# Optimization experiments

Hardware: AMD Instinct MI355X
Metric: run time of the kernel (lower is better)

Reference implementation:

```python
import jax, jax.numpy as jnp
import numpy as np

B, N, C = 8, 4096, 512
H = 8
OUT = 512
DH = C // H  # 64
LN_EPS = 1e-5
L2_EPS = 1e-12


def setup_inputs() -> dict:
    key = jax.random.key(0)
    ks = jax.random.split(key, 6)
    x = jax.random.normal(ks[0], (B, N, C), dtype=jnp.float32)
    ln_g = jnp.ones((C,), dtype=jnp.float32)
    ln_b = jnp.zeros((C,), dtype=jnp.float32)
    qkv_w = jax.random.normal(ks[1], (3 * C, C), dtype=jnp.float32) * 0.02  # torch Linear weight [out,in]
    temperature = jnp.ones((H, 1, 1), dtype=jnp.float32)
    proj_w = jax.random.normal(ks[2], (OUT, C), dtype=jnp.float32) * 0.02
    proj_b = jnp.zeros((OUT,), dtype=jnp.float32)
    return {"x": x, "ln_g": ln_g, "ln_b": ln_b, "qkv_w": qkv_w,
            "temperature": temperature, "proj_w": proj_w, "proj_b": proj_b}


def reference(x, ln_g, ln_b, qkv_w, temperature, proj_w, proj_b):
    # LayerNorm
    mu = jnp.mean(x, axis=-1, keepdims=True)
    var = jnp.mean(jnp.square(x - mu), axis=-1, keepdims=True)
    xn = (x - mu) * jax.lax.rsqrt(var + LN_EPS) * ln_g + ln_b
    # QKV projection (no bias)
    qkv = xn @ qkv_w.T  # [B,N,3C]
    qkv = qkv.reshape(B, N, 3, H, DH).transpose(2, 0, 3, 4, 1)  # [3,B,H,DH,N]
    q, k, v = qkv[0], qkv[1], qkv[2]  # each [B,H,DH,N] (already 'transposed' channel layout)
    # L2-normalize q,k along token dim (matches F.normalize eps behavior)
    q = q / jnp.clip(jnp.linalg.norm(q, axis=-1, keepdims=True), L2_EPS)
    k = k / jnp.clip(jnp.linalg.norm(k, axis=-1, keepdims=True), L2_EPS)
    # channel attention [B,H,DH,DH], scaled by per-head temperature
    attn = jnp.einsum('bhdn,bhen->bhde', q, k) * temperature[None]
    attn = jax.nn.softmax(attn, axis=-1)
    out = jnp.einsum('bhde,bhen->bhdn', attn, v)  # [B,H,DH,N]
    out = out.transpose(0, 3, 1, 2).reshape(B, N, H * DH)  # [B,N,C]
    out = jax.nn.gelu(out, approximate=False)
    out = out @ proj_w.T + proj_b
    return out
```

## Files before the change

### kernel.cpp

```cpp
#include <hip/hip_runtime.h>
#include <hip/hip_bf16.h>

typedef __hip_bfloat16 bf16;
typedef __bf16 bfrag __attribute__((ext_vector_type(8)));
typedef float f32x4 __attribute__((ext_vector_type(4)));

#define AS1 __attribute__((address_space(1)))
#define AS3 __attribute__((address_space(3)))

static constexpr int Bb = 8, Nn = 4096, Cc = 512, Hh = 8;
static constexpr int Mtok = Bb * Nn;
static constexpr int QKVC = 3 * Cc;
static constexpr size_t WS_NEED = 57147392;
static constexpr int SPL_STRIDE = 8 * 20 * 8192;

__device__ __forceinline__ void gl_lds16(const void* g, void* l) {
  __builtin_amdgcn_global_load_lds((const AS1 void*)g, (AS3 void*)l, 16, 0, 0);
}
__device__ __forceinline__ float gelu_exact(float x) {
  return 0.5f * x * (1.0f + erff(x * 0.70710678118654752f));
}
__device__ __forceinline__ int g3(int x) { return ((x & 1) << 2) | (x >> 1); }
__device__ __forceinline__ int tileid(int mt, int nt) {
  return mt + (nt == 0 ? 0 : nt == 1 ? 2 : nt == 2 ? 6 : 12);
}

__global__ __launch_bounds__(256) void fill_f32(float* o, float val, int n) {
  int i = blockIdx.x * 256 + threadIdx.x;
  if (i < n) o[i] = val;
}

__global__ __launch_bounds__(256) void ln_cvtw(const float* __restrict__ x,
                                               const float* __restrict__ gw,
                                               const float* __restrict__ bw,
                                               bf16* __restrict__ xn,
                                               const float* __restrict__ qkv_w,
                                               const float* __restrict__ proj_w,
                                               bf16* __restrict__ wq,
                                               bf16* __restrict__ wp) {
  int bid = blockIdx.x;
  if (bid < 8192) {
    int tok  = bid * 4 + (threadIdx.x >> 6);
    int lane = threadIdx.x & 63;
    const float* xr = x + (size_t)tok * Cc + lane * 8;
    float f[8];
    *(float4*)f       = *(const float4*)xr;
    *(float4*)(f + 4) = *(const float4*)(xr + 4);
    float s = 0.f;
#pragma unroll
    for (int j = 0; j < 8; ++j) s += f[j];
#pragma unroll
    for (int m = 32; m; m >>= 1) s += __shfl_xor(s, m);
    float mu = s * (1.0f / 512.0f);
    float q = 0.f;
#pragma unroll
    for (int j = 0; j < 8; ++j) { float d = f[j] - mu; q += d * d; }
#pragma unroll
    for (int m = 32; m; m >>= 1) q += __shfl_xor(q, m);
    float rstd = rsqrtf(q * (1.0f / 512.0f) + 1e-5f);
    bf16 o[8];
#pragma unroll
    for (int j = 0; j < 8; ++j)
      o[j] = __float2bfloat16((f[j] - mu) * rstd * gw[lane * 8 + j] + bw[lane * 8 + j]);
    *(uint4*)(xn + (size_t)tok * Cc + lane * 8) = *(uint4*)o;
  } else {
    int cb = bid - 8192;
    const float* a;
    bf16* o;
    int i;
    if (cb < 384) { a = qkv_w;  o = wq; i = (cb * 256 + (int)threadIdx.x) * 8; }
    else          { a = proj_w; o = wp; i = ((cb - 384) * 256 + (int)threadIdx.x) * 8; }
    float f[8];
    *(float4*)f       = *(const float4*)(a + i);
    *(float4*)(f + 4) = *(const float4*)(a + i + 4);
    bf16 vv[8];
#pragma unroll
    for (int j = 0; j < 8; ++j) vv[j] = __float2bfloat16(f[j]);
    *(uint4*)(o + i) = *(uint4*)vv;
  }
}

__global__ __launch_bounds__(256) void cvt_mirror(const float* __restrict__ part,
                                                  bf16* __restrict__ Gcvb) {
  int tile = blockIdx.x, b = blockIdx.y;
  int ti = tile >> 2, tj = tile & 3;
  int t = threadIdx.x;
  bf16* ob = Gcvb + (size_t)b * Cc * Cc;
  if (ti <= tj) {
#pragma unroll
    for (int r8 = 0; r8 < 8; ++r8) {
      int row = r8 * 16 + (t >> 4), col = (t & 15) * 8;
      int mt = 2 * ti + (row >> 6), rsub = row & 63;
      const float* p0 = part + ((size_t)b * 20 + tileid(mt, tj)) * 8192 + rsub * 128 + col;
      float f[8];
      *(float4*)f       = *(const float4*)p0;
      *(float4*)(f + 4) = *(const float4*)(p0 + 4);
#pragma unroll
      for (int s = 1; s < 4; ++s) {
        const float* ps = p0 + (size_t)s * SPL_STRIDE;
        float g[8];
        *(float4*)g       = *(const float4*)ps;
        *(float4*)(g + 4) = *(const float4*)(ps + 4);
#pragma unroll
        for (int j = 0; j < 8; ++j) f[j] += g[j];
      }
      bf16 v[8];
#pragma unroll
      for (int j = 0; j < 8; ++j) v[j] = __float2bfloat16(f[j]);
      *(uint4*)(ob + (size_t)(ti * 128 + row) * Cc + tj * 128 + col) = *(uint4*)v;
    }
  } else {
    __shared__ bf16 ls[128][136];
#pragma unroll
    for (int r8 = 0; r8 < 8; ++r8) {
      int srow = r8 * 16 + (t >> 4), scol = (t & 15) * 8;
      int mt = 2 * tj + (srow >> 6), rsub = srow & 63;
      const float* p0 = part + ((size_t)b * 20 + tileid(mt, ti)) * 8192 + rsub * 128 + scol;
      float f[8];
      *(float4*)f       = *(const float4*)p0;
      *(float4*)(f + 4) = *(const float4*)(p0 + 4);
#pragma unroll
      for (int s = 1; s < 4; ++s) {
        const float* ps = p0 + (size_t)s * SPL_STRIDE;
        float g[8];
        *(float4*)g       = *(const float4*)ps;
        *(float4*)(g + 4) = *(const float4*)(ps + 4);
#pragma unroll
        for (int j = 0; j < 8; ++j) f[j] += g[j];
      }
      bf16 v[8];
#pragma unroll
      for (int j = 0; j < 8; ++j) v[j] = __float2bfloat16(f[j]);
      *(uint4*)&ls[srow][scol] = *(uint4*)v;
    }
    __syncthreads();
#pragma unroll
    for (int r8 = 0; r8 < 8; ++r8) {
      int orow = r8 * 16 + (t >> 4), ocol = (t & 15) * 8;
      bf16 v[8];
#pragma unroll
      for (int u = 0; u < 8; ++u) v[u] = ls[ocol + u][orow];
      *(uint4*)(ob + (size_t)(ti * 128 + orow) * Cc + tj * 128 + ocol) = *(uint4*)v;
    }
  }
}

template <typename TC, bool SWZ>
__global__ __launch_bounds__(256) void gemm_bt(const bf16* __restrict__ A,
                                               const bf16* __restrict__ B,
                                               TC* __restrict__ C,
                                               int M, int N, int K,
                                               const float* __restrict__ bias,
                                               long sA_z, long sB_z, long sC_z) {
  A += (size_t)blockIdx.z * sA_z;
  B += (size_t)blockIdx.z * sB_z;
  C += (size_t)blockIdx.z * sC_z;
  __shared__ __align__(16) bf16 smem[16384];
  bf16* sA = smem;
  bf16* sB = smem + 8192;
  int t = threadIdx.x, w = t >> 6, lane = t & 63, fr = lane & 15, quad = lane >> 4;
  int n0, m0;
  if constexpr (SWZ) {
    int flat = blockIdx.y * 4 + blockIdx.x;
    int idx  = (flat & 7) * 128 + (flat >> 3);
    n0 = (idx & 3) * 128;
    m0 = (idx >> 2) * 128;
  } else {
    n0 = blockIdx.x * 128;
    m0 = blockIdx.y * 128;
  }
  int wm = (w >> 1) * 64, wn = (w & 1) * 64;
  f32x4 acc[4][4] = {};

  for (int k0 = 0; k0 < K; k0 += 64) {
    __syncthreads();
#pragma unroll
    for (int c2 = 0; c2 < 4; ++c2) {
      int c = w * 4 + c2;
      int row = c * 8 + (lane >> 3);
      int ke  = ((lane & 7) ^ (lane >> 3)) * 8;
      gl_lds16(A + (size_t)(m0 + row) * K + k0 + ke, (char*)sA + c * 1024);
      gl_lds16(B + (size_t)(n0 + row) * K + k0 + ke, (char*)sB + c * 1024);
    }
    __syncthreads();
#pragma unroll
    for (int kk = 0; kk < 64; kk += 32) {
      bfrag af[4], bg[4];
#pragma unroll
      for (int i = 0; i < 4; ++i)
        af[i] = *(const bfrag*)(sA + (wm + i * 16 + fr) * 64 +
                                ((((kk >> 3) + quad) ^ (fr & 7)) * 8));
#pragma unroll
      for (int j = 0; j < 4; ++j)
        bg[j] = *(const bfrag*)(sB + (wn + j * 16 + fr) * 64 +
                                ((((kk >> 3) + quad) ^ (fr & 7)) * 8));
#pragma unroll
      for (int i = 0; i < 4; ++i)
#pragma unroll
        for (int j = 0; j < 4; ++j)
          acc[i][j] = __builtin_amdgcn_mfma_f32_16x16x32_bf16(af[i], bg[j], acc[i][j], 0, 0, 0);
    }
  }

  if constexpr (__is_same(TC, float)) {
#pragma unroll
    for (int j = 0; j < 4; ++j) {
      float bj = bias ? bias[n0 + wn + j * 16 + fr] : 0.0f;
#pragma unroll
      for (int i = 0; i < 4; ++i)
#pragma unroll
        for (int r = 0; r < 4; ++r)
          C[(size_t)(m0 + wm + i * 16 + quad * 4 + r) * N + n0 + wn + j * 16 + fr] =
              acc[i][j][r] + bj;
    }
  } else {
    __syncthreads();
    bf16* ct = smem;
#pragma unroll
    for (int j = 0; j < 4; ++j) {
      float bj = bias ? bias[n0 + wn + j * 16 + fr] : 0.0f;
#pragma unroll
      for (int i = 0; i < 4; ++i)
#pragma unroll
        for (int r = 0; r < 4; ++r)
          ct[(wm + i * 16 + quad * 4 + r) * 128 + wn + j * 16 + fr] =
              __float2bfloat16(acc[i][j][r] + bj);
    }
    __syncthreads();
#pragma unroll
    for (int r8 = 0; r8 < 8; ++r8) {
      int row = r8 * 16 + (t >> 4);
      int ce  = (t & 15) * 8;
      *(uint4*)(C + (size_t)(m0 + row) * N + n0 + ce) = *(const uint4*)(smem + row * 128 + ce);
    }
  }
}

__global__ __launch_bounds__(256) void vgemm_xtx(const bf16* __restrict__ xn,
                                                 const bf16* __restrict__ wv,
                                                 bf16* __restrict__ v,
                                                 float* __restrict__ part) {
  __shared__ __align__(16) bf16 smem[16384];
  int t = threadIdx.x, w = t >> 6, lane = t & 63, fr = lane & 15, quad = lane >> 4;
  if (blockIdx.x < 1024) {
    bf16* sA = smem;
    bf16* sB = smem + 8192;
    int flat = blockIdx.x;
    int idx  = (flat & 7) * 128 + (flat >> 3);
    int n0 = (idx & 3) * 128, m0 = (idx >> 2) * 128;
    int wm = (w >> 1) * 64, wn = (w & 1) * 64;
    f32x4 acc[4][4] = {};
    for (int k0 = 0; k0 < 512; k0 += 64) {
      __syncthreads();
#pragma unroll
      for (int c2 = 0; c2 < 4; ++c2) {
        int c = w * 4 + c2;
        int row = c * 8 + (lane >> 3);
        int ke  = ((lane & 7) ^ (lane >> 3)) * 8;
        gl_lds16(xn + (size_t)(m0 + row) * 512 + k0 + ke, (char*)sA + c * 1024);
        gl_lds16(wv + (size_t)(n0 + row) * 512 + k0 + ke, (char*)sB + c * 1024);
      }
      __syncthreads();
#pragma unroll
      for (int kk = 0; kk < 64; kk += 32) {
        bfrag af[4], bg[4];
#pragma unroll
        for (int i = 0; i < 4; ++i)
          af[i] = *(const bfrag*)(sA + (wm + i * 16 + fr) * 64 +
                                  ((((kk >> 3) + quad) ^ (fr & 7)) * 8));
#pragma unroll
        for (int j = 0; j < 4; ++j)
          bg[j] = *(const bfrag*)(sB + (wn + j * 16 + fr) * 64 +
                                  ((((kk >> 3) + quad) ^ (fr & 7)) * 8));
#pragma unroll
        for (int i = 0; i < 4; ++i)
#pragma unroll
          for (int j = 0; j < 4; ++j)
            acc[i][j] = __builtin_amdgcn_mfma_f32_16x16x32_bf16(af[i], bg[j], acc[i][j], 0, 0, 0);
      }
    }
    __syncthreads();
    bf16* ct = smem;
#pragma unroll
    for (int j = 0; j < 4; ++j)
#pragma unroll
      for (int i = 0; i < 4; ++i)
#pragma unroll
        for (int r = 0; r < 4; ++r)
          ct[(wm + i * 16 + quad * 4 + r) * 128 + wn + j * 16 + fr] =
              __float2bfloat16(acc[i][j][r]);
    __syncthreads();
#pragma unroll
    for (int r8 = 0; r8 < 8; ++r8) {
      int row = r8 * 16 + (t >> 4);
      int ce  = (t & 15) * 8;
      *(uint4*)(v + (size_t)(m0 + row) * 512 + n0 + ce) = *(const uint4*)(smem + row * 128 + ce);
    }
  } else {
    bf16* sB  = smem;
    bf16* sAb = smem + 8192;
    int flat = blockIdx.x - 1024;
    int idx  = (flat & 7) * 80 + (flat >> 3);
    int tile = idx % 20;
    int sb   = idx / 20;
    int split = sb & 3, b = sb >> 2;
    int nt = tile < 2 ? 0 : tile < 6 ? 1 : tile < 12 ? 2 : 3;
    int mt = tile - (nt == 0 ? 0 : nt == 1 ? 2 : nt == 2 ? 6 : 12);
    int m0 = mt * 64, n0 = nt * 128;
    bool alias = ((mt >> 1) == nt);
    int wn = w * 32;
    bf16* sA = alias ? (sB + (mt & 1) * 4096) : sAb;
    f32x4 acc[4][2] = {};
    const bf16* xb = xn + ((size_t)b * Nn + split * 1024) * Cc;
    int ch0b = (t & 15) * 8, tgb = t >> 4;
    int ch0a = (t & 7) * 8,  tga = t >> 3;
    bool doA = (!alias) && (t < 128);
    unsigned swz = (unsigned)g3(t & 7);
    unsigned wposb = (((unsigned)(tgb >> 1) ^ swz) * 16u) + (unsigned)(tgb & 1) * 8u;
    unsigned wposa = (((unsigned)(tga >> 1) ^ swz) * 16u) + (unsigned)(tga & 1) * 8u;
    uint4 va[4], vb[4];
#pragma unroll
    for (int j = 0; j < 4; ++j)
      vb[j] = *(const uint4*)(xb + (size_t)(tgb * 4 + j) * Cc + n0 + ch0b);
    if (doA)
#pragma unroll
      for (int j = 0; j < 4; ++j)
        va[j] = *(const uint4*)(xb + (size_t)(tga * 4 + j) * Cc + m0 + ch0a);
    for (int kc = 0; kc < 16; ++kc) {
      __syncthreads();
#pragma unroll
      for (int k = 0; k < 4; ++k) {
        unsigned b0 = ((const unsigned*)&vb[0])[k], b1 = ((const unsigned*)&vb[1])[k];
        unsigned b2 = ((const unsigned*)&vb[2])[k], b3 = ((const unsigned*)&vb[3])[k];
        uint2 lo = { (b0 & 0xffffu) | (b1 << 16), (b2 & 0xffffu) | (b3 << 16) };
        uint2 hi = { (b0 >> 16) | (b1 & 0xffff0000u), (b2 >> 16) | (b3 & 0xffff0000u) };
        *(uint2*)((char*)sB + (unsigned)(ch0b + 2 * k) * 128 + wposb) = lo;
        *(uint2*)((char*)sB + (unsigned)(ch0b + 2 * k + 1) * 128 + wposb) = hi;
      }
      if (doA) {
#pragma unroll
        for (int k = 0; k < 4; ++k) {
          unsigned a0 = ((const unsigned*)&va[0])[k], a1 = ((const unsigned*)&va[1])[k];
          unsigned a2 = ((const unsigned*)&va[2])[k], a3 = ((const unsigned*)&va[3])[k];
          uint2 lo = { (a0 & 0xffffu) | (a1 << 16), (a2 & 0xffffu) | (a3 << 16) };
          uint2 hi = { (a0 >> 16) | (a1 & 0xffff0000u), (a2 >> 16) | (a3 & 0xffff0000u) };
          *(uint2*)((char*)sAb + (unsigned)(ch0a + 2 * k) * 128 + wposa) = lo;
          *(uint2*)((char*)sAb + (unsigned)(ch0a + 2 * k + 1) * 128 + wposa) = hi;
        }
      }
      __syncthreads();
      if (kc < 15) {
        const bf16* xb2 = xb + (size_t)(kc + 1) * 64 * Cc;
#pragma unroll
        for (int j = 0; j < 4; ++j)
          vb[j] = *(const uint4*)(xb2 + (size_t)(tgb * 4 + j) * Cc + n0 + ch0b);
        if (doA)
#pragma unroll
          for (int j = 0; j < 4; ++j)
            va[j] = *(const uint4*)(xb2 + (size_t)(tga * 4 + j) * Cc + m0 + ch0a);
      }
#pragma unroll
      for (int kk = 0; kk < 2; ++kk) {
        bfrag af[4], bg[2];
#pragma unroll
        for (int i = 0; i < 4; ++i) {
          int ch = i * 16 + fr;
          int slot = (kk * 4 + quad) ^ g3((ch >> 3) & 7);
          af[i] = *(const bfrag*)(sA + ch * 64 + slot * 8);
        }
#pragma unroll
        for (int j = 0; j < 2; ++j) {
          int ch = wn + j * 16 + fr;
          int slot = (kk * 4 + quad) ^ g3((ch >> 3) & 7);
          bg[j] = *(const bfrag*)(sB + ch * 64 + slot * 8);
        }
#pragma unroll
        for (int i = 0; i < 4; ++i)
#pragma unroll
          for (int j = 0; j < 2; ++j)
            acc[i][j] = __builtin_amdgcn_mfma_f32_16x16x32_bf16(af[i], bg[j], acc[i][j], 0, 0, 0);
      }
    }
    float* pb = part + (size_t)split * SPL_STRIDE + ((size_t)b * 20 + tile) * 8192;
#pragma unroll
    for (int i = 0; i < 4; ++i)
#pragma unroll
      for (int j = 0; j < 2; ++j)
#pragma unroll
        for (int r = 0; r < 4; ++r)
          pb[(i * 16 + quad * 4 + r) * 128 + wn + j * 16 + fr] = acc[i][j][r];
  }
}

__global__ __launch_bounds__(256) void gram_softmax(const bf16* __restrict__ T,
                                                    const bf16* __restrict__ wq,
                                                    const float* __restrict__ temp,
                                                    bf16* __restrict__ P) {
  int h = blockIdx.x, b = blockIdx.y;
  int t = threadIdx.x, w = t >> 6, lane = t & 63, fr = lane & 15, quad = lane >> 4;
  const bf16* Tq = T + (size_t)b * 1024 * 512 + (size_t)(h * 64) * 512;
  const bf16* Tk = T + (size_t)b * 1024 * 512 + (size_t)(512 + h * 64) * 512;
  const bf16* Wqh = wq + (size_t)(h * 64) * 512;
  const bf16* Wkh = wq + (size_t)(512 + h * 64) * 512;
  f32x4 acc[4][4] = {};
#pragma unroll
  for (int s = 0; s < 4; ++s) {
    int kb = w * 128 + s * 32 + quad * 8;
    bfrag af[4], bg[4];
#pragma unroll
    for (int i = 0; i < 4; ++i) af[i] = *(const bfrag*)(Tq + (size_t)(i * 16 + fr) * 512 + kb);
#pragma unroll
    for (int j = 0; j < 4; ++j) bg[j] = *(const bfrag*)(Wkh + (size_t)(j * 16 + fr) * 512 + kb);
#pragma unroll
    for (int i = 0; i < 4; ++i)
#pragma unroll
      for (int j = 0; j < 4; ++j)
        acc[i][j] = __builtin_amdgcn_mfma_f32_16x16x32_bf16(af[i], bg[j], acc[i][j], 0, 0, 0);
  }
  __shared__ float parts[4 * 4096];
  __shared__ float nrm[2][4][64];
  __shared__ float nqk[2][64];
#pragma unroll
  for (int i = 0; i < 4; ++i)
#pragma unroll
    for (int j = 0; j < 4; ++j)
#pragma unroll
      for (int r = 0; r < 4; ++r)
        parts[w * 4096 + (i * 16 + quad * 4 + r) * 64 + j * 16 + fr] = acc[i][j][r];
  {
    int d = t & 63, qtr = t >> 6, c0 = qtr * 128;
    float pq = 0.f, pk = 0.f;
#pragma unroll 4
    for (int cc = 0; cc < 16; ++cc) {
      bf16 a[8], ww[8];
      *(uint4*)a  = *(const uint4*)(Tq + (size_t)d * 512 + c0 + cc * 8);
      *(uint4*)ww = *(const uint4*)(Wqh + (size_t)d * 512 + c0 + cc * 8);
#pragma unroll
      for (int j = 0; j < 8; ++j) pq += __bfloat162float(a[j]) * __bfloat162float(ww[j]);
      *(uint4*)a  = *(const uint4*)(Tk + (size_t)d * 512 + c0 + cc * 8);
      *(uint4*)ww = *(const uint4*)(Wkh + (size_t)d * 512 + c0 + cc * 8);
#pragma unroll
      for (int j = 0; j < 8; ++j) pk += __bfloat162float(a[j]) * __bfloat162float(ww[j]);
    }
    nrm[0][qtr][d] = pq;
    nrm[1][qtr][d] = pk;
  }
  __syncthreads();
  if (t < 64) {
    nqk[0][t] = fmaxf(sqrtf(nrm[0][0][t] + nrm[0][1][t] + nrm[0][2][t] + nrm[0][3][t]), 1e-12f);
    nqk[1][t] = fmaxf(sqrtf(nrm[1][0][t] + nrm[1][1][t] + nrm[1][2][t] + nrm[1][3][t]), 1e-12f);
  }
  __syncthreads();
  if (t < 64) {
    int d = t;
    float sc = temp[h] / nqk[0][d];
    float l[64]; float mx = -1e30f;
#pragma unroll
    for (int e = 0; e < 64; ++e) {
      float vsum = parts[d * 64 + e] + parts[4096 + d * 64 + e] +
                   parts[8192 + d * 64 + e] + parts[12288 + d * 64 + e];
      l[e] = vsum * sc / nqk[1][e];
      mx = fmaxf(mx, l[e]);
    }
    float sum = 0.f;
#pragma unroll
    for (int e = 0; e < 64; ++e) { l[e] = expf(l[e] - mx); sum += l[e]; }
    float inv = 1.0f / sum;
    bf16* pr = P + ((size_t)(b * 8 + h) * 64 + d) * 64;
#pragma unroll
    for (int e = 0; e < 64; ++e) pr[e] = __float2bfloat16(l[e] * inv);
  }
}

__global__ __launch_bounds__(256) void pv_gelu(const bf16* __restrict__ P,
                                               const bf16* __restrict__ v,
                                               bf16* __restrict__ g) {
  int chunk = blockIdx.x, h = blockIdx.y, b = blockIdx.z;
  int t = threadIdx.x, w = t >> 6, lane = t & 63, fr = lane & 15, quad = lane >> 4;
  const bf16* pb = P + (size_t)(b * 8 + h) * 4096;
  bfrag pf[4][2];
#pragma unroll
  for (int i = 0; i < 4; ++i)
#pragma unroll
    for (int c = 0; c < 2; ++c)
      pf[i][c] = *(const bfrag*)(pb + (i * 16 + fr) * 64 + c * 32 + quad * 8);
#pragma unroll 2
  for (int nt = 0; nt < 8; ++nt) {
    int ntok = chunk * 512 + w * 128 + nt * 16 + fr;
    const bf16* vrow = v + (size_t)(b * Nn + ntok) * Cc + h * 64 + quad * 8;
    bfrag bv0 = *(const bfrag*)(vrow);
    bfrag bv1 = *(const bfrag*)(vrow + 32);
    f32x4 acc[4] = {};
#pragma unroll
    for (int i = 0; i < 4; ++i) {
      acc[i] = __builtin_amdgcn_mfma_f32_16x16x32_bf16(pf[i][0], bv0, acc[i], 0, 0, 0);
      acc[i] = __builtin_amdgcn_mfma_f32_16x16x32_bf16(pf[i][1], bv1, acc[i], 0, 0, 0);
    }
    bf16* grow = g + (size_t)(b * Nn + ntok) * Cc + h * 64;
#pragma unroll
    for (int i = 0; i < 4; ++i) {
      bf16 o[4];
#pragma unroll
      for (int r = 0; r < 4; ++r) o[r] = __float2bfloat16(gelu_exact(acc[i][r]));
      *(uint2*)(grow + i * 16 + quad * 4) = *(uint2*)o;
    }
  }
}

extern "C" void kernel_launch(void* const* d_in, const int* in_sizes, int n_in,
                              void* d_out, int out_size, void* d_ws, size_t ws_size,
                              hipStream_t stream) {
  const float* x      = (const float*)d_in[0];
  const float* ln_g   = (const float*)d_in[1];
  const float* ln_b   = (const float*)d_in[2];
  const float* qkv_w  = (const float*)d_in[3];
  const float* temp   = (const float*)d_in[4];
  const float* proj_w = (const float*)d_in[5];
  const float* proj_b = (const float*)d_in[6];
  float* out = (float*)d_out;
  char*  ws  = (char*)d_ws;

  const int exp_sizes[7] = {16777216, 512, 512, 786432, 8, 262144, 512};
  bool sizes_ok = (n_in == 7) && (out_size == 16777216);
  if (sizes_ok) for (int i = 0; i < 7; ++i) sizes_ok = sizes_ok && (in_sizes[i] == exp_sizes[i]);
  if (!sizes_ok) {
    fill_f32<<<(16777216 + 255) / 256, 256, 0, stream>>>(out, 500.0f, out_size);
    return;
  }
  if (ws_size < WS_NEED) {
    fill_f32<<<(16777216 + 255) / 256, 256, 0, stream>>>(out, (float)(ws_size >> 20), out_size);
    return;
  }

  bf16*  xn   = (bf16*)ws;
  bf16*  g    = (bf16*)ws;
  bf16*  Gcvb = (bf16*)(ws + 41943040);
  bf16*  T    = (bf16*)(ws + 46137344);
  bf16*  P    = (bf16*)(ws + 54525952);
  bf16*  wq   = (bf16*)(ws + 55050240);
  bf16*  wp   = (bf16*)(ws + 56623104);
  bf16*  v    = (bf16*)d_out;
  float* part = (float*)((char*)d_out + 33554432);

  ln_cvtw<<<8704, 256, 0, stream>>>(x, ln_g, ln_b, xn, qkv_w, proj_w, wq, wp);
  vgemm_xtx<<<1664, 256, 0, stream>>>(xn, wq + 1024 * 512, v, part);
  cvt_mirror<<<dim3(16, 8), 256, 0, stream>>>(part, Gcvb);
  gemm_bt<bf16, false><<<dim3(4, 8, 8), 256, 0, stream>>>(wq, Gcvb, T, 1024, Cc, Cc,
                                                          nullptr, 0, (long)Cc * Cc, (long)1024 * Cc);
  gram_softmax<<<dim3(Hh, Bb), 256, 0, stream>>>(T, wq, temp, P);
  pv_gelu<<<dim3(8, Hh, Bb), 256, 0, stream>>>(P, v, g);
  gemm_bt<float, true><<<dim3(4, 256, 1), 256, 0, stream>>>(g, wp, out, Mtok, Cc, Cc,
                                                            proj_b, 0, 0, 0);
}
```

Baseline: 258.1 us.

## Use 256x256 double-buffered GEMM for V and output projections, split xtx kernel

Adds a new GEMM kernel with 512 threads, 256x256 output tiles and double-buffered LDS staging using direct global-to-LDS loads. It is used for both the V projection and the final output projection. The fused V-GEMM/XtX kernel is split into two separate launches. Larger tiles raise arithmetic intensity and cut operand reloads, and overlapping the next tile's load with compute hides memory latency. In exchange, the 128 KB of LDS and the large accumulators allow only one block per CU, and the 256-block grid gives low occupancy and a tail effect.

Result: no change. 254.7 us (-1.3%).

```diff
diff --git a/kernel.cpp b/kernel.cpp
--- a/kernel.cpp
+++ b/kernel.cpp
@@ -236,160 +236,191 @@
   }
 }
 
-__global__ __launch_bounds__(256) void vgemm_xtx(const bf16* __restrict__ xn,
-                                                 const bf16* __restrict__ wv,
-                                                 bf16* __restrict__ v,
-                                                 float* __restrict__ part) {
-  __shared__ __align__(16) bf16 smem[16384];
+template <typename TC>
+__global__ __launch_bounds__(512) void gemm_bt2(const bf16* __restrict__ A,
+                                                const bf16* __restrict__ B,
+                                                TC* __restrict__ C,
+                                                int M, int N, int K,
+                                                const float* __restrict__ bias) {
+  __shared__ __align__(16) bf16 smem[65536];
   int t = threadIdx.x, w = t >> 6, lane = t & 63, fr = lane & 15, quad = lane >> 4;
-  if (blockIdx.x < 1024) {
-    bf16* sA = smem;
-    bf16* sB = smem + 8192;
-    int flat = blockIdx.x;
-    int idx  = (flat & 7) * 128 + (flat >> 3);
-    int n0 = (idx & 3) * 128, m0 = (idx >> 2) * 128;
-    int wm = (w >> 1) * 64, wn = (w & 1) * 64;
-    f32x4 acc[4][4] = {};
-    for (int k0 = 0; k0 < 512; k0 += 64) {
-      __syncthreads();
-#pragma unroll
-      for (int c2 = 0; c2 < 4; ++c2) {
-        int c = w * 4 + c2;
-        int row = c * 8 + (lane >> 3);
-        int ke  = ((lane & 7) ^ (lane >> 3)) * 8;
-        gl_lds16(xn + (size_t)(m0 + row) * 512 + k0 + ke, (char*)sA + c * 1024);
-        gl_lds16(wv + (size_t)(n0 + row) * 512 + k0 + ke, (char*)sB + c * 1024);
+  int nt2 = N >> 8;
+  int flat = blockIdx.x;
+  int idx  = (flat & 7) * (gridDim.x >> 3) + (flat >> 3);
+  int m0 = (idx / nt2) * 256, n0 = (idx % nt2) * 256;
+  int wm = (w >> 2) * 128, wn = (w & 3) * 64;
+  f32x4 acc[8][4] = {};
+
+  auto stage = [&](int buf, int k0) {
+    char* sAc = (char*)(smem + buf * 32768);
+    char* sBc = sAc + 32768;
+    int ke = ((lane & 7) ^ (lane >> 3)) * 8;
+#pragma unroll
+    for (int c2 = 0; c2 < 4; ++c2) {
+      int c = w * 4 + c2;
+      int row = c * 8 + (lane >> 3);
+      gl_lds16(A + (size_t)(m0 + row) * K + k0 + ke, sAc + c * 1024);
+      gl_lds16(B + (size_t)(n0 + row) * K + k0 + ke, sBc + c * 1024);
+    }
+  };
+
+  stage(0, 0);
+  __syncthreads();
+  int nks = K >> 6;
+  for (int ks = 0; ks < nks; ++ks) {
+    if (ks + 1 < nks) stage((ks + 1) & 1, (ks + 1) * 64);
+    const bf16* sA = smem + (ks & 1) * 32768;
+    const bf16* sB = sA + 16384;
+#pragma unroll
+    for (int kk = 0; kk < 64; kk += 32) {
+      bfrag af[8], bg[4];
+#pragma unroll
+      for (int i = 0; i < 8; ++i)
+        af[i] = *(const bfrag*)(sA + (wm + i * 16 + fr) * 64 +
+                                ((((kk >> 3) + quad) ^ (fr & 7)) * 8));
+#pragma unroll
+      for (int j = 0; j < 4; ++j)
+        bg[j] = *(const bfrag*)(sB + (wn + j * 16 + fr) * 64 +
+                                ((((kk >> 3) + quad) ^ (fr & 7)) * 8));
+#pragma unroll
+      for (int i = 0; i < 8; ++i)
+#pragma unroll
+        for (int j = 0; j < 4; ++j)
+          acc[i][j] = __builtin_amdgcn_mfma_f32_16x16x32_bf16(af[i], bg[j], acc[i][j], 0, 0, 0);
+    }
+    __syncthreads();
+  }
+
+  if constexpr (__is_same(TC, float)) {
+#pragma unroll
+    for (int j = 0; j < 4; ++j) {
+      float bj = bias ? bias[n0 + wn + j * 16 + fr] : 0.0f;
+#pragma unroll
+      for (int i = 0; i < 8; ++i)
+#pragma unroll
+        for (int r = 0; r < 4; ++r)
+          C[(size_t)(m0 + wm + i * 16 + quad * 4 + r) * N + n0 + wn + j * 16 + fr] =
+              acc[i][j][r] + bj;
+    }
+  } else {
+    bf16* ct = smem;
+#pragma unroll
+    for (int j = 0; j < 4; ++j) {
+      float bj = bias ? bias[n0 + wn + j * 16 + fr] : 0.0f;
+#pragma unroll
+      for (int i = 0; i < 8; ++i)
+#pragma unroll
+        for (int r = 0; r < 4; ++r)
+          ct[(wm + i * 16 + quad * 4 + r) * 256 + wn + j * 16 + fr] =
+              __float2bfloat16(acc[i][j][r] + bj);
+    }
+    __syncthreads();
+#pragma unroll
+    for (int it = 0; it < 16; ++it) {
+      int row = it * 16 + (t >> 5);
+      int ce  = (t & 31) * 8;
+      *(uint4*)(C + (size_t)(m0 + row) * N + n0 + ce) = *(const uint4*)(ct + row * 256 + ce);
+    }
+  }
+}
+
+__global__ __launch_bounds__(256) void xtx(const bf16* __restrict__ xn,
+                                           float* __restrict__ part) {
+  bf16* sB;
+  bf16* sAb;
+  __shared__ __align__(16) bf16 smem[12288];
+  sB = smem; sAb = smem + 8192;
+  int flat = blockIdx.x;
+  int idx  = (flat & 7) * 80 + (flat >> 3);
+  int tile = idx % 20;
+  int sb   = idx / 20;
+  int split = sb & 3, b = sb >> 2;
+  int nt = tile < 2 ? 0 : tile < 6 ? 1 : tile < 12 ? 2 : 3;
+  int mt = tile - (nt == 0 ? 0 : nt == 1 ? 2 : nt == 2 ? 6 : 12);
+  int m0 = mt * 64, n0 = nt * 128;
+  bool alias = ((mt >> 1) == nt);
+  int t = threadIdx.x, w = t >> 6, lane = t & 63, fr = lane & 15, quad = lane >> 4;
+  int wn = w * 32;
+  bf16* sA = alias ? (sB + (mt & 1) * 4096) : sAb;
+  f32x4 acc[4][2] = {};
+  const bf16* xb = xn + ((size_t)b * Nn + split * 1024) * Cc;
+  int ch0b = (t & 15) * 8, tgb = t >> 4;
+  int ch0a = (t & 7) * 8,  tga = t >> 3;
+  bool doA = (!alias) && (t < 128);
+  unsigned swz = (unsigned)g3(t & 7);
+  unsigned wposb = (((unsigned)(tgb >> 1) ^ swz) * 16u) + (unsigned)(tgb & 1) * 8u;
+  unsigned wposa = (((unsigned)(tga >> 1) ^ swz) * 16u) + (unsigned)(tga & 1) * 8u;
+  uint4 va[4], vb[4];
+#pragma unroll
+  for (int j = 0; j < 4; ++j)
+    vb[j] = *(const uint4*)(xb + (size_t)(tgb * 4 + j) * Cc + n0 + ch0b);
+  if (doA)
+#pragma unroll
+    for (int j = 0; j < 4; ++j)
+      va[j] = *(const uint4*)(xb + (size_t)(tga * 4 + j) * Cc + m0 + ch0a);
+  for (int kc = 0; kc < 16; ++kc) {
+    __syncthreads();
+#pragma unroll
+    for (int k = 0; k < 4; ++k) {
+      unsigned b0 = ((const unsigned*)&vb[0])[k], b1 = ((const unsigned*)&vb[1])[k];
+      unsigned b2 = ((const unsigned*)&vb[2])[k], b3 = ((const unsigned*)&vb[3])[k];
+      uint2 lo = { (b0 & 0xffffu) | (b1 << 16), (b2 & 0xffffu) | (b3 << 16) };
+      uint2 hi = { (b0 >> 16) | (b1 & 0xffff0000u), (b2 >> 16) | (b3 & 0xffff0000u) };
+      *(uint2*)((char*)sB + (unsigned)(ch0b + 2 * k) * 128 + wposb) = lo;
+      *(uint2*)((char*)sB + (unsigned)(ch0b + 2 * k + 1) * 128 + wposb) = hi;
+    }
+    if (doA) {
+#pragma unroll
+      for (int k = 0; k < 4; ++k) {
+        unsigned a0 = ((const unsigned*)&va[0])[k], a1 = ((const unsigned*)&va[1])[k];
+        unsigned a2 = ((const unsigned*)&va[2])[k], a3 = ((const unsigned*)&va[3])[k];
+        uint2 lo = { (a0 & 0xffffu) | (a1 << 16), (a2 & 0xffffu) | (a3 << 16) };
+        uint2 hi = { (a0 >> 16) | (a1 & 0xffff0000u), (a2 >> 16) | (a3 & 0xffff0000u) };
+        *(uint2*)((char*)sAb + (unsigned)(ch0a + 2 * k) * 128 + wposa) = lo;
+        *(uint2*)((char*)sAb + (unsigned)(ch0a + 2 * k + 1) * 128 + wposa) = hi;
       }
-      __syncthreads();
-#pragma unroll
-      for (int kk = 0; kk < 64; kk += 32) {
-        bfrag af[4], bg[4];
-#pragma unroll
-        for (int i = 0; i < 4; ++i)
-          af[i] = *(const bfrag*)(sA + (wm + i * 16 + fr) * 64 +
-                                  ((((kk >> 3) + quad) ^ (fr & 7)) * 8));
+    }
+    __syncthreads();
+    if (kc < 15) {
+      const bf16* xb2 = xb + (size_t)(kc + 1) * 64 * Cc;
+#pragma unroll
+      for (int j = 0; j < 4; ++j)
+        vb[j] = *(const uint4*)(xb2 + (size_t)(tgb * 4 + j) * Cc + n0 + ch0b);
+      if (doA)
 #pragma unroll
         for (int j = 0; j < 4; ++j)
-          bg[j] = *(const bfrag*)(sB + (wn + j * 16 + fr) * 64 +
-                                  ((((kk >> 3) + quad) ^ (fr & 7)) * 8));
-#pragma unroll
-        for (int i = 0; i < 4; ++i)
-#pragma unroll
-          for (int j = 0; j < 4; ++j)
-            acc[i][j] = __builtin_amdgcn_mfma_f32_16x16x32_bf16(af[i], bg[j], acc[i][j], 0, 0, 0);
+          va[j] = *(const uint4*)(xb2 + (size_t)(tga * 4 + j) * Cc + m0 + ch0a);
+    }
+#pragma unroll
+    for (int kk = 0; kk < 2; ++kk) {
+      bfrag af[4], bg[2];
+#pragma unroll
+      for (int i = 0; i < 4; ++i) {
+        int ch = i * 16 + fr;
+        int slot = (kk * 4 + quad) ^ g3((ch >> 3) & 7);
+        af[i] = *(const bfrag*)(sA + ch * 64 + slot * 8);
       }
-    }
-    __syncthreads();
-    bf16* ct = smem;
-#pragma unroll
-    for (int j = 0; j < 4; ++j)
+#pragma unroll
+      for (int j = 0; j < 2; ++j) {
+        int ch = wn + j * 16 + fr;
+        int slot = (kk * 4 + quad) ^ g3((ch >> 3) & 7);
+        bg[j] = *(const bfrag*)(sB + ch * 64 + slot * 8);
+      }
 #pragma unroll
       for (int i = 0; i < 4; ++i)
 #pragma unroll
-        for (int r = 0; r < 4; ++r)
-          ct[(wm + i * 16 + quad * 4 + r) * 128 + wn + j * 16 + fr] =
-              __float2bfloat16(acc[i][j][r]);
-    __syncthreads();
-#pragma unroll
-    for (int r8 = 0; r8 < 8; ++r8) {
-      int row = r8 * 16 + (t >> 4);
-      int ce  = (t & 15) * 8;
-      *(uint4*)(v + (size_t)(m0 + row) * 512 + n0 + ce) = *(const uint4*)(smem + row * 128 + ce);
-    }
-  } else {
-    bf16* sB  = smem;
-    bf16* sAb = smem + 8192;
-    int flat = blockIdx.x - 1024;
-    int idx  = (flat & 7) * 80 + (flat >> 3);
-    int tile = idx % 20;
-    int sb   = idx / 20;
-    int split = sb & 3, b = sb >> 2;
-    int nt = tile < 2 ? 0 : tile < 6 ? 1 : tile < 12 ? 2 : 3;
-    int mt = tile - (nt == 0 ? 0 : nt == 1 ? 2 : nt == 2 ? 6 : 12);
-    int m0 = mt * 64, n0 = nt * 128;
-    bool alias = ((mt >> 1) == nt);
-    int wn = w * 32;
-    bf16* sA = alias ? (sB + (mt & 1) * 4096) : sAb;
-    f32x4 acc[4][2] = {};
-    const bf16* xb = xn + ((size_t)b * Nn + split * 1024) * Cc;
-    int ch0b = (t & 15) * 8, tgb = t >> 4;
-    int ch0a = (t & 7) * 8,  tga = t >> 3;
-    bool doA = (!alias) && (t < 128);
-    unsigned swz = (unsigned)g3(t & 7);
-    unsigned wposb = (((unsigned)(tgb >> 1) ^ swz) * 16u) + (unsigned)(tgb & 1) * 8u;
-    unsigned wposa = (((unsigned)(tga >> 1) ^ swz) * 16u) + (unsigned)(tga & 1) * 8u;
-    uint4 va[4], vb[4];
-#pragma unroll
-    for (int j = 0; j < 4; ++j)
-      vb[j] = *(const uint4*)(xb + (size_t)(tgb * 4 + j) * Cc + n0 + ch0b);
-    if (doA)
-#pragma unroll
-      for (int j = 0; j < 4; ++j)
-        va[j] = *(const uint4*)(xb + (size_t)(tga * 4 + j) * Cc + m0 + ch0a);
-    for (int kc = 0; kc < 16; ++kc) {
-      __syncthreads();
-#pragma unroll
-      for (int k = 0; k < 4; ++k) {
-        unsigned b0 = ((const unsigned*)&vb[0])[k], b1 = ((const unsigned*)&vb[1])[k];
-        unsigned b2 = ((const unsigned*)&vb[2])[k], b3 = ((const unsigned*)&vb[3])[k];
-        uint2 lo = { (b0 & 0xffffu) | (b1 << 16), (b2 & 0xffffu) | (b3 << 16) };
-        uint2 hi = { (b0 >> 16) | (b1 & 0xffff0000u), (b2 >> 16) | (b3 & 0xffff0000u) };
-        *(uint2*)((char*)sB + (unsigned)(ch0b + 2 * k) * 128 + wposb) = lo;
-        *(uint2*)((char*)sB + (unsigned)(ch0b + 2 * k + 1) * 128 + wposb) = hi;
-      }
-      if (doA) {
-#pragma unroll
-        for (int k = 0; k < 4; ++k) {
-          unsigned a0 = ((const unsigned*)&va[0])[k], a1 = ((const unsigned*)&va[1])[k];
-          unsigned a2 = ((const unsigned*)&va[2])[k], a3 = ((const unsigned*)&va[3])[k];
-          uint2 lo = { (a0 & 0xffffu) | (a1 << 16), (a2 & 0xffffu) | (a3 << 16) };
-          uint2 hi = { (a0 >> 16) | (a1 & 0xffff0000u), (a2 >> 16) | (a3 & 0xffff0000u) };
-          *(uint2*)((char*)sAb + (unsigned)(ch0a + 2 * k) * 128 + wposa) = lo;
-          *(uint2*)((char*)sAb + (unsigned)(ch0a + 2 * k + 1) * 128 + wposa) = hi;
-        }
-      }
-      __syncthreads();
-      if (kc < 15) {
-        const bf16* xb2 = xb + (size_t)(kc + 1) * 64 * Cc;
-#pragma unroll
-        for (int j = 0; j < 4; ++j)
-          vb[j] = *(const uint4*)(xb2 + (size_t)(tgb * 4 + j) * Cc + n0 + ch0b);
-        if (doA)
-#pragma unroll
-          for (int j = 0; j < 4; ++j)
-            va[j] = *(const uint4*)(xb2 + (size_t)(tga * 4 + j) * Cc + m0 + ch0a);
-      }
-#pragma unroll
-      for (int kk = 0; kk < 2; ++kk) {
-        bfrag af[4], bg[2];
-#pragma unroll
-        for (int i = 0; i < 4; ++i) {
-          int ch = i * 16 + fr;
-          int slot = (kk * 4 + quad) ^ g3((ch >> 3) & 7);
-          af[i] = *(const bfrag*)(sA + ch * 64 + slot * 8);
-        }
-#pragma unroll
-        for (int j = 0; j < 2; ++j) {
-          int ch = wn + j * 16 + fr;
-          int slot = (kk * 4 + quad) ^ g3((ch >> 3) & 7);
-          bg[j] = *(const bfrag*)(sB + ch * 64 + slot * 8);
-        }
-#pragma unroll
-        for (int i = 0; i < 4; ++i)
-#pragma unroll
-          for (int j = 0; j < 2; ++j)
-            acc[i][j] = __builtin_amdgcn_mfma_f32_16x16x32_bf16(af[i], bg[j], acc[i][j], 0, 0, 0);
-      }
-    }
-    float* pb = part + (size_t)split * SPL_STRIDE + ((size_t)b * 20 + tile) * 8192;
-#pragma unroll
-    for (int i = 0; i < 4; ++i)
-#pragma unroll
-      for (int j = 0; j < 2; ++j)
-#pragma unroll
-        for (int r = 0; r < 4; ++r)
-          pb[(i * 16 + quad * 4 + r) * 128 + wn + j * 16 + fr] = acc[i][j][r];
-  }
+        for (int j = 0; j < 2; ++j)
+          acc[i][j] = __builtin_amdgcn_mfma_f32_16x16x32_bf16(af[i], bg[j], acc[i][j], 0, 0, 0);
+    }
+  }
+  float* pb = part + (size_t)split * SPL_STRIDE + ((size_t)b * 20 + tile) * 8192;
+#pragma unroll
+  for (int i = 0; i < 4; ++i)
+#pragma unroll
+    for (int j = 0; j < 2; ++j)
+#pragma unroll
+      for (int r = 0; r < 4; ++r)
+        pb[(i * 16 + quad * 4 + r) * 128 + wn + j * 16 + fr] = acc[i][j][r];
 }
 
 __global__ __launch_bounds__(256) void gram_softmax(const bf16* __restrict__ T,
@@ -543,12 +574,12 @@
   float* part = (float*)((char*)d_out + 33554432);
 
   ln_cvtw<<<8704, 256, 0, stream>>>(x, ln_g, ln_b, xn, qkv_w, proj_w, wq, wp);
-  vgemm_xtx<<<1664, 256, 0, stream>>>(xn, wq + 1024 * 512, v, part);
+  gemm_bt2<bf16><<<256, 512, 0, stream>>>(xn, wq + 1024 * 512, v, Mtok, Cc, Cc, nullptr);
+  xtx<<<640, 256, 0, stream>>>(xn, part);
   cvt_mirror<<<dim3(16, 8), 256, 0, stream>>>(part, Gcvb);
   gemm_bt<bf16, false><<<dim3(4, 8, 8), 256, 0, stream>>>(wq, Gcvb, T, 1024, Cc, Cc,
                                                           nullptr, 0, (long)Cc * Cc, (long)1024 * Cc);
   gram_softmax<<<dim3(Hh, Bb), 256, 0, stream>>>(T, wq, temp, P);
   pv_gelu<<<dim3(8, Hh, Bb), 256, 0, stream>>>(P, v, g);
-  gemm_bt<float, true><<<dim3(4, 256, 1), 256, 0, stream>>>(g, wp, out, Mtok, Cc, Cc,
-                                                            proj_b, 0, 0, 0);
-}
+  gemm_bt2<float><<<256, 512, 0, stream>>>(g, wp, out, Mtok, Cc, Cc, proj_b);
+}
```
